# Kernel optimization log

Hardware: AMD Instinct MI355X
Metric: run time of the kernel (lower is better)

Reference implementation:

```python
import jax, jax.numpy as jnp
import numpy as np


def _conv(x, w, b=None, stride=1, pad=0):
    # x: [N,C,H,W], w: [O,I,kh,kw]
    out = jax.lax.conv_general_dilated(
        x, w, (stride, stride), [(pad, pad), (pad, pad)],
        dimension_numbers=('NCHW', 'OIHW', 'NCHW'))
    return out if b is None else out + b[None, :, None, None]


def _cond_net(x, cw1, cb1, cw2, cb2, cw3, cb3):
    # ZeroPad2d(1) + conv(pad=0) == conv(pad=1)
    h = jax.nn.relu(_conv(x, cw1, cb1, stride=2, pad=1))
    h = jax.nn.relu(_conv(h, cw2, cb2, stride=2, pad=1))
    h = jax.nn.relu(_conv(h, cw3, cb3, stride=2, pad=1))
    return h.mean(axis=(2, 3))  # [B, 32]


def _hda(x, dyn_w, ow, share_w, share_b):
    # per-sample dynamic conv: weight[b] = dyn_w * ow[b]
    B = x.shape[0]
    w = dyn_w[None] * ow.reshape(B, *dyn_w.shape)  # [B,32,64,3,3]
    out1 = jax.vmap(lambda xb, wb: _conv(xb[None], wb, pad=1)[0])(x, w)
    out2 = _conv(x, share_w, share_b, pad=1)
    return jnp.concatenate([out1, out2], axis=1)  # [B,64,H,W]


def setup_inputs() -> dict:
    key = jax.random.key(0)
    ks = jax.random.split(key, 20)
    s = 0.05
    inp = {
        'x': jax.random.normal(ks[0], (8, 64, 256, 256), jnp.float32),
        'out_weight1': jax.random.normal(ks[1], (256, 64, 3, 3), jnp.float32),
        'out_weight2': jax.random.normal(ks[2], (256, 64, 3, 3), jnp.float32),
        # Condition_tp params
        'cw1': jax.random.normal(ks[3], (32, 64, 7, 7), jnp.float32) * s,
        'cb1': jnp.zeros((32,), jnp.float32),
        'cw2': jax.random.normal(ks[4], (32, 32, 3, 3), jnp.float32) * s,
        'cb2': jnp.zeros((32,), jnp.float32),
        'cw3': jax.random.normal(ks[5], (32, 32, 3, 3), jnp.float32) * s,
        'cb3': jnp.zeros((32,), jnp.float32),
        # FiLM linears (cond_nf=32 -> base_nf=64)
        'scale_w': jax.random.normal(ks[6], (64, 32), jnp.float32) * s,
        'scale_b': jnp.zeros((64,), jnp.float32),
        'shift_w': jax.random.normal(ks[7], (64, 32), jnp.float32) * s,
        'shift_b': jnp.zeros((64,), jnp.float32),
        # HDA_conv 1
        'dyn1_w': jax.random.normal(ks[8], (32, 64, 3, 3), jnp.float32) * s,
        'share1_w': jax.random.normal(ks[9], (32, 64, 3, 3), jnp.float32) * s,
        'share1_b': jnp.zeros((32,), jnp.float32),
        # HDA_conv 2
        'dyn2_w': jax.random.normal(ks[10], (32, 64, 3, 3), jnp.float32) * s,
        'share2_w': jax.random.normal(ks[11], (32, 64, 3, 3), jnp.float32) * s,
        'share2_b': jnp.zeros((32,), jnp.float32),
    }
    return inp


def reference(x, out_weight1, out_weight2, cw1, cb1, cw2, cb2, cw3, cb3,
              scale_w, scale_b, shift_w, shift_b,
              dyn1_w, share1_w, share1_b, dyn2_w, share2_w, share2_b):
    res_scale = 1.0
    cond = _cond_net(x, cw1, cb1, cw2, cb2, cw3, cb3)       # [B,32]
    scale = cond @ scale_w.T + scale_b                      # [B,64]
    shift = cond @ shift_w.T + shift_b                      # [B,64]
    out = _hda(x, dyn1_w, out_weight1, share1_w, share1_b)  # [B,64,H,W]
    # out*scale + shift + out  ==  out*(scale+1) + shift
    out = out * (scale[:, :, None, None] + 1.0) + shift[:, :, None, None]
    out = jax.nn.relu(out)
    out = _hda(out, dyn2_w, out_weight2, share2_w, share2_b)
    return x + out * res_scale
```

## Files before the change

kernel.cpp:

```cpp
#include <hip/hip_runtime.h>

typedef unsigned short u16;
typedef unsigned int u32;
typedef __attribute__((ext_vector_type(8))) __bf16 bf16x8;
typedef __attribute__((ext_vector_type(8))) u16 u16x8;
typedef __attribute__((ext_vector_type(4))) float f32x4;
typedef __attribute__((ext_vector_type(2))) u32 u32x2;

static constexpr size_t PSP = (size_t)8 * 258 * 258 * 16;

#define GPTR(p) ((const __attribute__((address_space(1))) void*)(p))
#define LPTR(p) ((__attribute__((address_space(3))) void*)(p))

__device__ __forceinline__ u16 f2bf(float f) {
  u32 u = __builtin_bit_cast(u32, f);
  u = (u + 0x7FFFu + ((u >> 16) & 1u)) >> 16;
  return (u16)u;
}

__device__ __forceinline__ f32x4 mfma16(bf16x8 a, bf16x8 b, f32x4 c) {
  return __builtin_amdgcn_mfma_f32_16x16x32_bf16(a, b, c, 0, 0, 0);
}

__global__ void k_zero_border(u16* __restrict__ base) {
  int idx = blockIdx.x * 256 + threadIdx.x;
  if (idx >= 4 * 8 * 1028) return;
  int p = idx / (8 * 1028), r = idx - p * (8 * 1028);
  int b = r / 1028, e = r - b * 1028;
  int y, x;
  if (e < 258) { y = 0; x = e; }
  else if (e < 516) { y = 257; x = e - 258; }
  else { int e2 = e - 516; y = 1 + (e2 >> 1); x = (e2 & 1) * 257; }
  u16* d = base + (size_t)p * PSP + (((size_t)b * 258 + y) * 258 + x) * 16;
  u16x8 z = (u16x8)0;
  *(u16x8*)d = z;
  *(u16x8*)(d + 8) = z;
}

__global__ __launch_bounds__(256) void k_tr(const float* __restrict__ x,
                                            u16* __restrict__ xh) {
  __shared__ float t[64][33];
  const int b = blockIdx.z, y = blockIdx.y, x0 = blockIdx.x * 32;
  const int tid = threadIdx.x;
  {
    int ic = tid >> 2, xo = (tid & 3) * 8;
    const float* s = x + (((size_t)b * 64 + ic) * 256 + y) * 256 + x0 + xo;
    f32x4 v0 = *(const f32x4*)s;
    f32x4 v1 = *(const f32x4*)(s + 4);
#pragma unroll
    for (int j = 0; j < 4; ++j) { t[ic][xo + j] = v0[j]; t[ic][xo + 4 + j] = v1[j]; }
  }
  __syncthreads();
  {
    int xc = tid & 31, slot = tid >> 5;
    int ic0 = slot * 8;
    u16x8 v;
#pragma unroll
    for (int j = 0; j < 8; ++j) v[j] = f2bf(t[ic0 + j][xc]);
    *(u16x8*)(xh + (size_t)(slot >> 1) * PSP +
              (((size_t)b * 258 + y + 1) * 258 + x0 + xc + 1) * 16 + (slot & 1) * 8) = v;
  }
}

__global__ void k_prep_cw(const float* __restrict__ src, u16* __restrict__ dst,
                          int IC, int KK2, int n, int perm) {
  int d = blockIdx.x * 256 + threadIdx.x;
  if (d >= n) return;
  int per = KK2 * IC;
  int oc = d / per, r = d - oc * per;
  int tap = r / IC, icp = r - tap * IC;
  int ic = perm ? ((icp >> 1) + (icp & 1) * 16) : icp;
  dst[d] = f2bf(src[(oc * IC + ic) * KK2 + tap]);
}

__global__ void k_prep_cw1(const float* __restrict__ src, u16* __restrict__ dst) {
  int d = blockIdx.x * 256 + threadIdx.x;
  if (d >= 106496) return;
  int h = d / 13312, r = d - h * 13312;
  int t = r >> 8, r2 = r & 255;
  int oc = r2 >> 3, i = r2 & 7;
  float v = (t < 49) ? src[(oc * 64 + h * 8 + i) * 49 + t] : 0.f;
  dst[d] = f2bf(v);
}

__global__ void k_prep_hda(const float* __restrict__ dyn, const float* __restrict__ ow,
                           const float* __restrict__ share, const float* __restrict__ a_,
                           u16* __restrict__ dst, int use_a, int perm) {
  int d = blockIdx.x * 256 + threadIdx.x;
  if (d >= 327680) return;
  int b = d / 40960, r = d - b * 40960;
  int cc = r / 10240, r2 = r - cc * 10240;
  int oc = r2 / 160, r3 = r2 - oc * 160;
  int s = r3 >> 5, r4 = r3 & 31;
  int kq = r4 >> 3, j = r4 & 7;
  int tap = 2 * s + (kq >> 1);
  float v = 0.f;
  if (tap < 9) {
    int icp = cc * 16 + (kq & 1) * 8 + j;
    int ic = perm ? ((icp & 3) * 16 + (icp >> 2)) : icp;
    v = (oc < 32) ? dyn[(oc * 64 + ic) * 9 + tap] * ow[((b * 32 + oc) * 64 + ic) * 9 + tap]
                  : share[((oc - 32) * 64 + ic) * 9 + tap];
    if (use_a) v *= a_[b * 64 + oc];
  }
  dst[d] = f2bf(v);
}

__global__ __launch_bounds__(256, 2) void k_cond1_mfma(const u16* __restrict__ xh,
    const u16* __restrict__ wp , const float* __restrict__ cb,
    u16* __restrict__ dst) {
  __shared__ char lds[49152];
  const int wg0 = blockIdx.x;
  const int wg = ((wg0 & 7) << 6) | (wg0 >> 3);
  const int b = wg >> 6, rr = wg & 63;
  const int oh0 = (rr >> 3) << 4, ow0 = (rr & 7) << 4;
  const int tid = threadIdx.x, lane = tid & 63, wid = tid >> 6;
  const int col = lane & 15, kq = lane >> 4;
  f32x4 acc[4][2];
#pragma unroll
  for (int i = 0; i < 4; ++i)
#pragma unroll
    for (int j = 0; j < 2; ++j) acc[i][j] = 0.f;
  int pb[4];
#pragma unroll
  for (int mf = 0; mf < 4; ++mf) pb[mf] = (2 * (wid * 4 + mf)) * 37 + 2 * col;
#pragma unroll 1
  for (int h = 0; h < 8; ++h) {
    __syncthreads();
#pragma unroll
    for (int it = 0; it < 6; ++it) {
      if (it < 5 || wid < 2) {
        int g = it * 256 + tid;
        int i = g ^ ((g >> 3) & 7);
        if (i >= 1406) i = 0;
        int r = i / 37, cc2 = i - r * 37;
        const u16* src = xh + (size_t)(h >> 1) * PSP +
            (((size_t)b * 258 + 2 * oh0 + r) * 258 + 2 * ow0 + cc2) * 16 + (h & 1) * 8;
        __builtin_amdgcn_global_load_lds(GPTR(src),
            LPTR(lds + (it * 256 + wid * 64) * 16), 16, 0, 0);
      }
    }
#pragma unroll
    for (int it = 0; it < 7; ++it) {
      if (it < 6 || wid < 2) {
        int g = it * 256 + tid;
        int t = g >> 5, oc = g & 31;
        const u16* src = wp + h * 13312 + t * 256 + oc * 8;
        __builtin_amdgcn_global_load_lds(GPTR(src),
            LPTR(lds + 22528 + (it * 256 + wid * 64) * 16), 16, 0, 0);
      }
    }
    __syncthreads();
    __builtin_amdgcn_s_setprio(1);
#pragma unroll
    for (int s = 0; s < 13; ++s) {
      const int t0 = 4 * s;
      const int kh0 = t0 / 7, r7 = t0 % 7;
      int carry = (kq >= 7 - r7) ? 1 : 0;
      int kh = kh0 + carry;
      int kw = r7 + kq - carry * 7;
      int prow = kh * 37 + kw;
      bf16x8 a[4];
#pragma unroll
      for (int mf = 0; mf < 4; ++mf) {
        int pos = pb[mf] + prow;
        int g = pos ^ ((pos >> 3) & 7);
        a[mf] = __builtin_bit_cast(bf16x8, *(const u16x8*)(lds + g * 16));
      }
      bf16x8 w[2];
#pragma unroll
      for (int nf = 0; nf < 2; ++nf)
        w[nf] = __builtin_bit_cast(bf16x8,
            *(const u16x8*)(lds + 22528 + (((4 * s + kq) * 32) + nf * 16 + col) * 16));
#pragma unroll
      for (int mf = 0; mf < 4; ++mf)
#pragma unroll
        for (int nf = 0; nf < 2; ++nf) acc[mf][nf] = mfma16(a[mf], w[nf], acc[mf][nf]);
    }
    __builtin_amdgcn_s_setprio(0);
  }
  const float bv0 = cb[col], bv1 = cb[16 + col];
#pragma unroll
  for (int mf = 0; mf < 4; ++mf) {
    int oh = oh0 + wid * 4 + mf;
    if (oh >= 126) continue;
#pragma unroll
    for (int r = 0; r < 4; ++r) {
      int ow = ow0 + kq * 4 + r;
      if (ow >= 126) continue;
      u32 pack = (u32)f2bf(fmaxf(acc[mf][0][r] + bv0, 0.f)) |
                 ((u32)f2bf(fmaxf(acc[mf][1][r] + bv1, 0.f)) << 16);
      *(u32*)(dst + (((size_t)b * 126 + oh) * 126 + ow) * 32 + col * 2) = pack;
    }
  }
}

template <int HI, int HO, int IC, int KK, int OUTF32>
__global__ __launch_bounds__(256, 4) void k_conv_s2(const u16* __restrict__ src,
    const u16* __restrict__ wgt, const float* __restrict__ bias, void* __restrict__ dst) {
  const int b = blockIdx.z;
  const int by0 = blockIdx.y * 8, bx0 = blockIdx.x * 16;
  const int tid = threadIdx.x, lane = tid & 63, wid = tid >> 6;
  const int col = lane & 15, kq = lane >> 4;
  f32x4 acc[2][2];
#pragma unroll
  for (int i = 0; i < 2; ++i)
#pragma unroll
    for (int j = 0; j < 2; ++j) acc[i][j] = 0.f;
  const u16x8 Z = (u16x8)0;
#pragma unroll
  for (int kh = 0; kh < KK; ++kh) {
#pragma unroll
    for (int kw = 0; kw < KK; ++kw) {
#pragma unroll
      for (int h = 0; h < IC / 32; ++h) {
        bf16x8 a[2];
#pragma unroll
        for (int mf = 0; mf < 2; ++mf) {
          int oh = by0 + wid * 2 + mf;
          int ih = 2 * oh - 1 + kh;
          int ix = 2 * (bx0 + col) - 1 + kw;
          int ic = h * 32 + kq * 8;
          u16x8 raw = Z;
          if ((unsigned)ih < (unsigned)HI && (unsigned)ix < (unsigned)HI)
            raw = *(const u16x8*)(src + (((size_t)b * HI + ih) * HI + ix) * IC + ic);
          a[mf] = __builtin_bit_cast(bf16x8, raw);
        }
        int k0 = (kh * KK + kw) * IC + h * 32 + kq * 8;
        bf16x8 w[2];
#pragma unroll
        for (int nf = 0; nf < 2; ++nf)
          w[nf] = __builtin_bit_cast(bf16x8,
                    *(const u16x8*)(wgt + (size_t)(nf * 16 + col) * (KK * KK * IC) + k0));
#pragma unroll
        for (int mf = 0; mf < 2; ++mf)
#pragma unroll
          for (int nf = 0; nf < 2; ++nf) acc[mf][nf] = mfma16(a[mf], w[nf], acc[mf][nf]);
      }
    }
  }
#pragma unroll
  for (int mf = 0; mf < 2; ++mf) {
    int oh = by0 + wid * 2 + mf;
    if (oh >= HO) continue;
#pragma unroll
    for (int nf = 0; nf < 2; ++nf) {
      int oc = nf * 16 + col;
      float bv = bias[oc];
#pragma unroll
      for (int r = 0; r < 4; ++r) {
        int ow = bx0 + kq * 4 + r;
        if (ow >= HO) continue;
        float v = fmaxf(acc[mf][nf][r] + bv, 0.f);
        if (OUTF32)
          ((float*)dst)[(((size_t)b * 32 + oc) * HO + oh) * HO + ow] = v;
        else
          ((u16*)dst)[(((size_t)b * HO + oh) * HO + ow) * 32 + oc] = f2bf(v);
      }
    }
  }
}

__global__ void k_mean(const float* __restrict__ h3, float* __restrict__ cond) {
  int bo = blockIdx.x;
  int tid = threadIdx.x;
  float s = 0.f;
  for (int i = tid; i < 1024; i += 256) s += h3[bo * 1024 + i];
  __shared__ float red[256];
  red[tid] = s;
  __syncthreads();
  for (int o = 128; o > 0; o >>= 1) {
    if (tid < o) red[tid] += red[tid + o];
    __syncthreads();
  }
  if (tid == 0) cond[bo] = red[0] * (1.f / 1024.f);
}

__global__ void k_film(const float* __restrict__ cond,
                       const float* __restrict__ scale_w, const float* __restrict__ scale_b,
                       const float* __restrict__ shift_w, const float* __restrict__ shift_b,
                       const float* __restrict__ share1_b, const float* __restrict__ share2_b,
                       float* __restrict__ a_, float* __restrict__ bias1,
                       float* __restrict__ bias2) {
  int t = threadIdx.x;
  int b = t >> 6, j = t & 63;
  float s = scale_b[j], sh = shift_b[j];
  for (int k = 0; k < 32; ++k) {
    float c = cond[b * 32 + k];
    s = fmaf(c, scale_w[j * 32 + k], s);
    sh = fmaf(c, shift_w[j * 32 + k], sh);
  }
  float a = s + 1.f;
  float b0 = (j < 32) ? 0.f : share1_b[j - 32];
  a_[t] = a;
  bias1[t] = fmaf(a, b0, sh);
  bias2[t] = (j < 32) ? 0.f : share2_b[j - 32];
}

__device__ __forceinline__ void hda_stage(const u16* __restrict__ asrc,
                                          const u16* __restrict__ wall,
                                          char* lb, int b, int by0, int bx0,
                                          int cc, int tid, int wid, int lane) {
  const u16* ap = asrc + (size_t)cc * PSP;
  const u16* wp = wall + (size_t)b * 40960 + cc * 10240;
#pragma unroll
  for (int it = 0; it < 3; ++it) {
    if (it < 2 || wid < 3) {
      int g = it * 256 + tid;
      int i = g ^ ((g >> 3) & 1);
      int pos = i >> 1, sl = i & 1;
      if (pos >= 342) { pos = 0; sl = 0; }
      int yy = pos / 18, xx = pos - yy * 18;
      const u16* src = ap + (((size_t)b * 258 + by0 + yy) * 258 + bx0 + xx) * 16 + sl * 8;
      __builtin_amdgcn_global_load_lds(GPTR(src), LPTR(lb + (it * 256 + wid * 64) * 16),
                                       16, 0, 0);
    }
  }
  for (int j = wid; j < 21; j += 4) {
    int gr = j * 64 + lane;
    int oc = gr / 21, t = gr - oc * 21;
    if (t > 19) t = 19;
    const u16* src = wp + oc * 160 + t * 8;
    __builtin_amdgcn_global_load_lds(GPTR(src), LPTR(lb + 11264 + j * 1024), 16, 0, 0);
  }
}

template <int STAGE>
__global__ __launch_bounds__(256, 2) void k_hda_mfma(const u16* __restrict__ asrc,
    const u16* __restrict__ wall, const float* __restrict__ bias,
    const float* __restrict__ resid, void* __restrict__ dst) {
  __shared__ char lds[65536];
  const int wg0 = blockIdx.x;
  const int wg = ((wg0 & 7) << 8) + (wg0 >> 3);
  const int b = wg >> 8;
  const int rr = wg & 255;
  const int by0 = (rr >> 4) << 4, bx0 = (rr & 15) << 4;
  const int tid = threadIdx.x, lane = tid & 63, wid = tid >> 6;
  const int col = lane & 15, kq = lane >> 4;
  const int hi = kq >> 1, sl2 = kq & 1;
  f32x4 acc[4][4];
#pragma unroll
  for (int i = 0; i < 4; ++i)
#pragma unroll
    for (int j = 0; j < 4; ++j) acc[i][j] = 0.f;
  hda_stage(asrc, wall, lds, b, by0, bx0, 0, tid, wid, lane);
#pragma unroll
  for (int cc = 0; cc < 4; ++cc) {
    __syncthreads();
    if (cc < 3)
      hda_stage(asrc, wall, lds + ((cc + 1) & 1) * 32768, b, by0, bx0, cc + 1,
                tid, wid, lane);
    char* lb = lds + (cc & 1) * 32768;
    __builtin_amdgcn_s_setprio(1);
#pragma unroll
    for (int s = 0; s < 5; ++s) {
      const int t0 = 2 * s, t1 = 2 * s + 1;
      const int d0 = (t0 / 3) * 18 + (t0 % 3);
      const int d1 = (t1 / 3) * 18 + (t1 % 3);
      const int dd = hi ? d1 : d0;
      bf16x8 a[4];
#pragma unroll
      for (int mf = 0; mf < 4; ++mf) {
        int pos = (wid * 4 + mf) * 18 + col + dd;
        int g = (pos * 2 + sl2) ^ ((pos >> 2) & 1);
        a[mf] = __builtin_bit_cast(bf16x8, *(const u16x8*)(lb + g * 16));
      }
      bf16x8 w[4];
#pragma unroll
      for (int nf = 0; nf < 4; ++nf)
        w[nf] = __builtin_bit_cast(bf16x8,
            *(const u16x8*)(lb + 11264 + (nf * 16 + col) * 336 + (s * 4 + kq) * 16));
#pragma unroll
      for (int mf = 0; mf < 4; ++mf)
#pragma unroll
        for (int nf = 0; nf < 4; ++nf) acc[mf][nf] = mfma16(a[mf], w[nf], acc[mf][nf]);
    }
    __builtin_amdgcn_s_setprio(0);
  }
  const float* bb = bias + b * 64;
#pragma unroll
  for (int mf = 0; mf < 4; ++mf) {
    int y = by0 + wid * 4 + mf;
    if (STAGE == 1) {
#pragma unroll
      for (int r = 0; r < 4; ++r) {
        int x = bx0 + kq * 4 + r;
        u32x2 pk;
        pk[0] = (u32)f2bf(fmaxf(acc[mf][0][r] + bb[col], 0.f)) |
                ((u32)f2bf(fmaxf(acc[mf][1][r] + bb[16 + col], 0.f)) << 16);
        pk[1] = (u32)f2bf(fmaxf(acc[mf][2][r] + bb[32 + col], 0.f)) |
                ((u32)f2bf(fmaxf(acc[mf][3][r] + bb[48 + col], 0.f)) << 16);
        *(u32x2*)((u16*)dst + (size_t)(col >> 2) * PSP +
                  (((size_t)b * 258 + y + 1) * 258 + x + 1) * 16 + (col & 3) * 4) = pk;
      }
    } else {
#pragma unroll
      for (int nf = 0; nf < 4; ++nf) {
        int oc = nf * 16 + col;
        float bv = bb[oc];
        size_t o = (((size_t)b * 64 + oc) * 256 + y) * 256 + bx0 + kq * 4;
        f32x4 rx = *(const f32x4*)(resid + o);
        f32x4 vv;
#pragma unroll
        for (int r = 0; r < 4; ++r) vv[r] = rx[r] + acc[mf][nf][r] + bv;
        *(f32x4*)((float*)dst + o) = vv;
      }
    }
  }
}

extern "C" void kernel_launch(void* const* d_in, const int* in_sizes, int n_in,
                              void* d_out, int out_size, void* d_ws, size_t ws_size,
                              hipStream_t stream) {
  const float* x        = (const float*)d_in[0];
  const float* ow1      = (const float*)d_in[1];
  const float* ow2      = (const float*)d_in[2];
  const float* cw1      = (const float*)d_in[3];
  const float* cb1      = (const float*)d_in[4];
  const float* cw2      = (const float*)d_in[5];
  const float* cb2      = (const float*)d_in[6];
  const float* cw3      = (const float*)d_in[7];
  const float* cb3      = (const float*)d_in[8];
  const float* scale_w  = (const float*)d_in[9];
  const float* scale_b  = (const float*)d_in[10];
  const float* shift_w  = (const float*)d_in[11];
  const float* shift_b  = (const float*)d_in[12];
  const float* dyn1     = (const float*)d_in[13];
  const float* share1   = (const float*)d_in[14];
  const float* share1_b = (const float*)d_in[15];
  const float* dyn2     = (const float*)d_in[16];
  const float* share2   = (const float*)d_in[17];
  const float* share2_b = (const float*)d_in[18];
  float* out = (float*)d_out;

  char* p = (char*)d_ws;
  u16* xh   = (u16*)p;            p += PSP * 4 * 2;
  u16* midh = (u16*)p;            p += PSP * 4 * 2;
  u16* wbf1 = (u16*)p;            p += (size_t)327680 * 2;
  u16* wbf2 = (u16*)p;            p += (size_t)327680 * 2;
  u16* cwb1 = (u16*)p;            p += (size_t)106496 * 2;
  u16* cwb2 = (u16*)p;            p += (size_t)32 * 288 * 2;
  u16* cwb3 = (u16*)p;            p += (size_t)32 * 288 * 2;
  float* a_    = (float*)p;       p += 512 * 4;
  float* bias1 = (float*)p;       p += 512 * 4;
  float* bias2 = (float*)p;       p += 512 * 4;
  float* cond  = (float*)p;       p += 256 * 4;
  u16* h1h = midh;
  u16* h2h = h1h + (size_t)8 * 126 * 126 * 32;
  float* h3 = (float*)(h2h + (size_t)8 * 63 * 63 * 32);

  k_zero_border<<<129, 256, 0, stream>>>(xh);
  k_tr<<<dim3(8, 256, 8), 256, 0, stream>>>(x, xh);

  k_prep_cw1<<<(106496 + 255) / 256, 256, 0, stream>>>(cw1, cwb1);
  k_prep_cw<<<(32 * 288 + 255) / 256, 256, 0, stream>>>(cw2, cwb2, 32, 9, 32 * 288, 1);
  k_prep_cw<<<(32 * 288 + 255) / 256, 256, 0, stream>>>(cw3, cwb3, 32, 9, 32 * 288, 0);

  k_cond1_mfma<<<512, 256, 0, stream>>>(xh, cwb1, cb1, h1h);
  k_conv_s2<126, 63, 32, 3, 0><<<dim3(4, 8, 8), 256, 0, stream>>>(h1h, cwb2, cb2, h2h);
  k_conv_s2<63, 32, 32, 3, 1><<<dim3(2, 4, 8), 256, 0, stream>>>(h2h, cwb3, cb3, h3);

  k_mean<<<256, 256, 0, stream>>>(h3, cond);
  k_film<<<1, 512, 0, stream>>>(cond, scale_w, scale_b, shift_w, shift_b,
                                share1_b, share2_b, a_, bias1, bias2);

  k_zero_border<<<129, 256, 0, stream>>>(midh);

  k_prep_hda<<<(327680 + 255) / 256, 256, 0, stream>>>(dyn1, ow1, share1, a_, wbf1, 1, 0);
  k_prep_hda<<<(327680 + 255) / 256, 256, 0, stream>>>(dyn2, ow2, share2, a_, wbf2, 0, 1);

  k_hda_mfma<1><<<2048, 256, 0, stream>>>(xh, wbf1, bias1, nullptr, midh);
  k_hda_mfma<2><<<2048, 256, 0, stream>>>(midh, wbf2, bias2, x, out);
}
```

Baseline: 251.3 us.

## Double HDA conv tile height and relayout weights for contiguous LDS staging

The HDA conv kernel now covers a 32x16 output tile per workgroup instead of 16x16, with each wave computing 8 rows. Each staged weight slice is therefore reused across twice as many pixels, and the halo overhead per output pixel drops. The prep kernel reorders weights as [tap-group][oc][8], so the weight copy into LDS becomes a plain contiguous load without the per-oc padded layout. The costs are more LDS (about 80KB with two buffers), twice the accumulator registers, and half as many workgroups, which may hurt occupancy or latency hiding. The old padded weight layout had a stride of 336 bytes, and the new contiguous one may bring LDS bank conflicts on the weight reads.

```diff
diff --git a/kernel.cpp b/kernel.cpp
--- a/kernel.cpp
+++ b/kernel.cpp
@@ -90,9 +90,9 @@
   if (d >= 327680) return;
   int b = d / 40960, r = d - b * 40960;
   int cc = r / 10240, r2 = r - cc * 10240;
-  int oc = r2 / 160, r3 = r2 - oc * 160;
-  int s = r3 >> 5, r4 = r3 & 31;
-  int kq = r4 >> 3, j = r4 & 7;
+  int t = r2 / 512, r3 = r2 - t * 512;
+  int oc = r3 >> 3, j = r3 & 7;
+  int s = t >> 2, kq = t & 3;
   int tap = 2 * s + (kq >> 1);
   float v = 0.f;
   if (tap < 9) {
@@ -299,28 +299,25 @@
 __device__ __forceinline__ void hda_stage(const u16* __restrict__ asrc,
                                           const u16* __restrict__ wall,
                                           char* lb, int b, int by0, int bx0,
-                                          int cc, int tid, int wid, int lane) {
+                                          int cc, int tid) {
   const u16* ap = asrc + (size_t)cc * PSP;
   const u16* wp = wall + (size_t)b * 40960 + cc * 10240;
 #pragma unroll
-  for (int it = 0; it < 3; ++it) {
-    if (it < 2 || wid < 3) {
+  for (int it = 0; it < 5; ++it) {
+    if (it < 4 || tid < 200) {
       int g = it * 256 + tid;
       int i = g ^ ((g >> 3) & 1);
       int pos = i >> 1, sl = i & 1;
-      if (pos >= 342) { pos = 0; sl = 0; }
+      if (pos >= 612) { pos = 0; sl = 0; }
       int yy = pos / 18, xx = pos - yy * 18;
       const u16* src = ap + (((size_t)b * 258 + by0 + yy) * 258 + bx0 + xx) * 16 + sl * 8;
-      __builtin_amdgcn_global_load_lds(GPTR(src), LPTR(lb + (it * 256 + wid * 64) * 16),
-                                       16, 0, 0);
-    }
-  }
-  for (int j = wid; j < 21; j += 4) {
-    int gr = j * 64 + lane;
-    int oc = gr / 21, t = gr - oc * 21;
-    if (t > 19) t = 19;
-    const u16* src = wp + oc * 160 + t * 8;
-    __builtin_amdgcn_global_load_lds(GPTR(src), LPTR(lb + 11264 + j * 1024), 16, 0, 0);
+      __builtin_amdgcn_global_load_lds(GPTR(src), LPTR(lb + g * 16), 16, 0, 0);
+    }
+  }
+#pragma unroll
+  for (int it = 0; it < 5; ++it) {
+    int g = it * 256 + tid;
+    __builtin_amdgcn_global_load_lds(GPTR(wp + g * 8), LPTR(lb + 19584 + g * 16), 16, 0, 0);
   }
 }
 
@@ -328,28 +325,27 @@
 __global__ __launch_bounds__(256, 2) void k_hda_mfma(const u16* __restrict__ asrc,
     const u16* __restrict__ wall, const float* __restrict__ bias,
     const float* __restrict__ resid, void* __restrict__ dst) {
-  __shared__ char lds[65536];
+  __shared__ char lds[80128];
   const int wg0 = blockIdx.x;
-  const int wg = ((wg0 & 7) << 8) + (wg0 >> 3);
-  const int b = wg >> 8;
-  const int rr = wg & 255;
-  const int by0 = (rr >> 4) << 4, bx0 = (rr & 15) << 4;
+  const int wg = ((wg0 & 7) << 7) | (wg0 >> 3);
+  const int b = wg >> 7;
+  const int rr = wg & 127;
+  const int by0 = (rr >> 4) * 32, bx0 = (rr & 15) * 16;
   const int tid = threadIdx.x, lane = tid & 63, wid = tid >> 6;
   const int col = lane & 15, kq = lane >> 4;
   const int hi = kq >> 1, sl2 = kq & 1;
-  f32x4 acc[4][4];
-#pragma unroll
-  for (int i = 0; i < 4; ++i)
+  f32x4 acc[8][4];
+#pragma unroll
+  for (int i = 0; i < 8; ++i)
 #pragma unroll
     for (int j = 0; j < 4; ++j) acc[i][j] = 0.f;
-  hda_stage(asrc, wall, lds, b, by0, bx0, 0, tid, wid, lane);
+  hda_stage(asrc, wall, lds, b, by0, bx0, 0, tid);
 #pragma unroll
   for (int cc = 0; cc < 4; ++cc) {
     __syncthreads();
     if (cc < 3)
-      hda_stage(asrc, wall, lds + ((cc + 1) & 1) * 32768, b, by0, bx0, cc + 1,
-                tid, wid, lane);
-    char* lb = lds + (cc & 1) * 32768;
+      hda_stage(asrc, wall, lds + ((cc + 1) & 1) * 40064, b, by0, bx0, cc + 1, tid);
+    const char* lb = lds + (cc & 1) * 40064;
     __builtin_amdgcn_s_setprio(1);
 #pragma unroll
     for (int s = 0; s < 5; ++s) {
@@ -357,10 +353,10 @@
       const int d0 = (t0 / 3) * 18 + (t0 % 3);
       const int d1 = (t1 / 3) * 18 + (t1 % 3);
       const int dd = hi ? d1 : d0;
-      bf16x8 a[4];
-#pragma unroll
-      for (int mf = 0; mf < 4; ++mf) {
-        int pos = (wid * 4 + mf) * 18 + col + dd;
+      bf16x8 a[8];
+#pragma unroll
+      for (int mf = 0; mf < 8; ++mf) {
+        int pos = (wid * 8 + mf) * 18 + col + dd;
         int g = (pos * 2 + sl2) ^ ((pos >> 2) & 1);
         a[mf] = __builtin_bit_cast(bf16x8, *(const u16x8*)(lb + g * 16));
       }
@@ -368,9 +364,9 @@
 #pragma unroll
       for (int nf = 0; nf < 4; ++nf)
         w[nf] = __builtin_bit_cast(bf16x8,
-            *(const u16x8*)(lb + 11264 + (nf * 16 + col) * 336 + (s * 4 + kq) * 16));
-#pragma unroll
-      for (int mf = 0; mf < 4; ++mf)
+            *(const u16x8*)(lb + 19584 + ((s * 4 + kq) * 64 + nf * 16 + col) * 16));
+#pragma unroll
+      for (int mf = 0; mf < 8; ++mf)
 #pragma unroll
         for (int nf = 0; nf < 4; ++nf) acc[mf][nf] = mfma16(a[mf], w[nf], acc[mf][nf]);
     }
@@ -378,8 +374,8 @@
   }
   const float* bb = bias + b * 64;
 #pragma unroll
-  for (int mf = 0; mf < 4; ++mf) {
-    int y = by0 + wid * 4 + mf;
+  for (int mf = 0; mf < 8; ++mf) {
+    int y = by0 + wid * 8 + mf;
     if (STAGE == 1) {
 #pragma unroll
       for (int r = 0; r < 4; ++r) {
@@ -468,6 +464,6 @@
   k_prep_hda<<<(327680 + 255) / 256, 256, 0, stream>>>(dyn1, ow1, share1, a_, wbf1, 1, 0);
   k_prep_hda<<<(327680 + 255) / 256, 256, 0, stream>>>(dyn2, ow2, share2, a_, wbf2, 0, 1);
 
-  k_hda_mfma<1><<<2048, 256, 0, stream>>>(xh, wbf1, bias1, nullptr, midh);
-  k_hda_mfma<2><<<2048, 256, 0, stream>>>(midh, wbf2, bias2, x, out);
-}
+  k_hda_mfma<1><<<1024, 256, 0, stream>>>(xh, wbf1, bias1, nullptr, midh);
+  k_hda_mfma<2><<<1024, 256, 0, stream>>>(midh, wbf2, bias2, x, out);
+}
```

Result: slower. 282.9 us (+12.6%).
